# Performance work log

Measured on AMD Instinct MI355X. Metric: run time of the kernel, lower is better.

Reference implementation:

```python
import jax, jax.numpy as jnp
import numpy as np

MODEL_DIM = 1024
NUM_HEADS = 16
K_DIM = MODEL_DIM // NUM_HEADS


def setup_inputs() -> dict:
    key = jax.random.key(0)
    kx, kw1, kw2 = jax.random.split(key, 3)
    B, L, D = 4, 2048, MODEL_DIM
    x = jax.random.normal(kx, (B, L, D), dtype=jnp.float32)
    # nn.Linear(D, 3D, bias=False): y = x @ W^T; store transposed form [D, 3D]
    scale1 = 1.0 / np.sqrt(D)
    Wqkv = jax.random.uniform(kw1, (D, 3 * D), dtype=jnp.float32, minval=-scale1, maxval=scale1)
    Wout = jax.random.uniform(kw2, (D, D), dtype=jnp.float32, minval=-scale1, maxval=scale1)
    return {"x": x, "Wqkv": Wqkv, "Wout": Wout}


def reference(x, Wqkv, Wout):
    B, L, D = x.shape
    H, Kd = NUM_HEADS, K_DIM
    qkv = x @ Wqkv  # [B, L, 3D]
    q, k, v = jnp.split(qkv, 3, axis=-1)

    def heads(t):  # [B, L, D] -> [B, H, L, Kd]
        return t.reshape(B, L, H, Kd).transpose(0, 2, 1, 3)

    qh, kh, vh = heads(q), heads(k), heads(v)
    scores = jnp.einsum('bhqd,bhkd->bhqk', qh, kh) / jnp.sqrt(jnp.float32(Kd))
    causal = jnp.triu(jnp.ones((L, L), dtype=bool), k=1)  # True above diagonal
    scores = jnp.where(causal, -jnp.inf, scores)
    probs = jax.nn.softmax(scores, axis=-1)
    attended = jnp.einsum('bhqk,bhkd->bhqd', probs, vh)
    concatted = attended.transpose(0, 2, 1, 3).reshape(B, L, D)
    # dropout is identity in eval mode
    return concatted @ Wout
```

## Files before the change

kernel.cpp:

```cpp
#include <hip/hip_runtime.h>

typedef unsigned short u16;
typedef unsigned int   u32;
typedef __bf16   bf16x8 __attribute__((ext_vector_type(8)));
typedef float    f32x4  __attribute__((ext_vector_type(4)));
typedef u16      u16x4  __attribute__((ext_vector_type(4)));
typedef u16      u16x8  __attribute__((ext_vector_type(8)));
typedef u32      u32x2  __attribute__((ext_vector_type(2)));
typedef u32      u32x4  __attribute__((ext_vector_type(4)));

#if __has_builtin(__builtin_amdgcn_exp2f)
#define EXP2(x) __builtin_amdgcn_exp2f(x)
#else
#define EXP2(x) exp2f(x)
#endif

__device__ __forceinline__ u16 f2bf(float f) {
    unsigned u = __float_as_uint(f);
    u += 0x7FFFu + ((u >> 16) & 1u);
    return (u16)(u >> 16);
}

__device__ __forceinline__ u32 pack_bf16(float a, float b) {
#if __has_builtin(__builtin_amdgcn_cvt_pk_bf16_f32)
    typedef __bf16 bf16x2 __attribute__((ext_vector_type(2)));
    bf16x2 r = __builtin_amdgcn_cvt_pk_bf16_f32(a, b);
    return __builtin_bit_cast(u32, r);
#else
    return (u32)f2bf(a) | ((u32)f2bf(b) << 16);
#endif
}

__device__ __forceinline__ void async_copy16(const u16* g, u16* l) {
    __builtin_amdgcn_global_load_lds(
        (const __attribute__((address_space(1))) unsigned*)g,
        (__attribute__((address_space(3))) unsigned*)l, 16, 0, 0);
}

__device__ __forceinline__ bf16x8 lds_frag(const u16* p) {
    return *(const bf16x8*)p;
}

__device__ __forceinline__ void permlane32_swap(u32& a, u32& b) {
    asm("v_permlane32_swap_b32 %0, %1" : "+v"(a), "+v"(b));
}
__device__ __forceinline__ void permlane16_swap(u32& a, u32& b) {
    asm("v_permlane16_swap_b32 %0, %1" : "+v"(a), "+v"(b));
}

__global__ __launch_bounds__(256) void prep(const float* __restrict__ x,
                                            const float* __restrict__ Wqkv,
                                            const float* __restrict__ Wout,
                                            u16* __restrict__ xb,
                                            u16* __restrict__ wqkv_t,
                                            u16* __restrict__ wout_t) {
    __shared__ u16 t[64 * 72];
    const int bid = blockIdx.x;
    const int tid = threadIdx.x;

    if (bid >= 1024) {
        size_t i = ((size_t)(bid - 1024) * 256 + tid) * 8;
        float4 v0 = *(const float4*)(x + i);
        float4 v1 = *(const float4*)(x + i + 4);
        u16x8 o = { f2bf(v0.x), f2bf(v0.y), f2bf(v0.z), f2bf(v0.w),
                    f2bf(v1.x), f2bf(v1.y), f2bf(v1.z), f2bf(v1.w) };
        *(u16x8*)(xb + i) = o;
        return;
    }

    const float* W;  u16* Wt;  int Kd, Nd, n0, k0;
    if (bid < 768) { W = Wqkv; Wt = wqkv_t; Kd = 1024; Nd = 3072;
                     n0 = (bid % 48) * 64; k0 = (bid / 48) * 64; }
    else           { W = Wout; Wt = wout_t; Kd = 1024; Nd = 1024;
                     n0 = ((bid - 768) % 16) * 64; k0 = ((bid - 768) / 16) * 64; }
#pragma unroll
    for (int i = 0; i < 4; ++i) {
        int lin = i * 256 + tid;
        int kr = lin >> 4, nc = (lin & 15) << 2;
        float4 v = *(const float4*)(W + (size_t)(k0 + kr) * Nd + n0 + nc);
        u16x4 o = { f2bf(v.x), f2bf(v.y), f2bf(v.z), f2bf(v.w) };
        *(u16x4*)&t[kr * 72 + nc] = o;
    }
    __syncthreads();
#pragma unroll
    for (int i = 0; i < 2; ++i) {
        int lin = i * 256 + tid;
        int nr = lin >> 3, kc = (lin & 7) << 3;
        u16x8 o;
#pragma unroll
        for (int jj = 0; jj < 8; ++jj) o[jj] = t[(kc + jj) * 72 + nr];
        *(u16x8*)(Wt + (size_t)(n0 + nr) * Kd + k0 + kc) = o;
    }
}

__global__ __launch_bounds__(256) void gemm_qkv(const u16* __restrict__ A,
                                                const u16* __restrict__ Bt,
                                                u16* __restrict__ outb,
                                                int K, int N) {
    __shared__ u16 As[2][128 * 32];
    __shared__ u16 Bs[2][128 * 32];
    const int tid = threadIdx.x;
    const int lane = tid & 63;
    const int wv = tid >> 6;
    const int wr = (wv >> 1) * 64;
    const int wc = (wv & 1) * 64;
    const int qd = lane >> 4;
    const int c  = lane & 15;
    const int m0 = blockIdx.y * 128;
    const int n0 = blockIdx.x * 128;

    const int srow = tid >> 2;
    const int sg = ((tid & 3) ^ ((srow >> 1) & 3)) << 3;

    const u16* Ag0 = A  + (size_t)(m0 +      srow) * K + sg;
    const u16* Ag1 = A  + (size_t)(m0 + 64 + srow) * K + sg;
    const u16* Bg0 = Bt + (size_t)(n0 +      srow) * K + sg;
    const u16* Bg1 = Bt + (size_t)(n0 + 64 + srow) * K + sg;

    const u32 fsw = (qd ^ ((c >> 1) & 3)) << 3;
    const u32 a_off = (wr + c) * 32 + fsw;
    const u32 b_off = (wc + c) * 32 + fsw;

    f32x4 acc[4][4] = {};

    async_copy16(Ag0, &As[0][tid * 8]);
    async_copy16(Ag1, &As[0][2048 + tid * 8]);
    async_copy16(Bg0, &Bs[0][tid * 8]);
    async_copy16(Bg1, &Bs[0][2048 + tid * 8]);

    int p = 0;
    for (int k0 = 0; k0 < K; k0 += 32) {
        __syncthreads();
        if (k0 + 32 < K) {
            const int np = p ^ 1;
            async_copy16(Ag0 + k0 + 32, &As[np][tid * 8]);
            async_copy16(Ag1 + k0 + 32, &As[np][2048 + tid * 8]);
            async_copy16(Bg0 + k0 + 32, &Bs[np][tid * 8]);
            async_copy16(Bg1 + k0 + 32, &Bs[np][2048 + tid * 8]);
        }
        bf16x8 af[4], bfr[4];
#pragma unroll
        for (int i = 0; i < 4; ++i) af[i]  = lds_frag(&As[p][a_off + i * 512]);
#pragma unroll
        for (int j = 0; j < 4; ++j) bfr[j] = lds_frag(&Bs[p][b_off + j * 512]);
#pragma unroll
        for (int i = 0; i < 4; ++i)
#pragma unroll
            for (int j = 0; j < 4; ++j)
                acc[i][j] = __builtin_amdgcn_mfma_f32_16x16x32_bf16(af[i], bfr[j], acc[i][j], 0, 0, 0);
        p ^= 1;
    }

#pragma unroll
    for (int i = 0; i < 4; ++i)
#pragma unroll
        for (int j = 0; j < 4; ++j) {
            int n = n0 + wc + j * 16 + c;
            int which = n >> 10, h = (n >> 6) & 15, kd = n & 63;
            int m_base = m0 + wr + i * 16 + qd * 4;
            int b = m_base >> 11, l0 = m_base & 2047;
            int bh = b * 16 + h;
            if (which == 2) {
                u32x2 o2;
                o2[0] = pack_bf16(acc[i][j][0], acc[i][j][1]);
                o2[1] = pack_bf16(acc[i][j][2], acc[i][j][3]);
                *(u32x2*)(outb + (size_t)(128 + bh) * 131072 + (size_t)kd * 2048 + l0) = o2;
            } else if (which == 0) {
#pragma unroll
                for (int r = 0; r < 4; ++r)
                    outb[(size_t)bh * 131072 + (size_t)(l0 + r) * 64 + kd] =
                        f2bf(acc[i][j][r] * 0.1803368801f);
            } else {
#pragma unroll
                for (int r = 0; r < 4; ++r)
                    outb[(size_t)(64 + bh) * 131072 + (size_t)(l0 + r) * 64 + kd] =
                        f2bf(acc[i][j][r]);
            }
        }
}

__global__ __launch_bounds__(256) void gemm_out(const u16* __restrict__ A,
                                                const u16* __restrict__ Bt,
                                                float* __restrict__ outf,
                                                int K, int N) {
    __shared__ u16 As[2][64 * 32];
    __shared__ u16 Bs[2][128 * 32];
    const int tid = threadIdx.x;
    const int lane = tid & 63;
    const int wv = tid >> 6;
    const int wr = (wv >> 1) * 32;
    const int wc = (wv & 1) * 64;
    const int qd = lane >> 4;
    const int c  = lane & 15;
    const int m0 = blockIdx.y * 64;
    const int n0 = blockIdx.x * 128;

    const int srow = tid >> 2;
    const int sg = ((tid & 3) ^ ((srow >> 1) & 3)) << 3;

    const u16* Ag0 = A  + (size_t)(m0 +      srow) * K + sg;
    const u16* Bg0 = Bt + (size_t)(n0 +      srow) * K + sg;
    const u16* Bg1 = Bt + (size_t)(n0 + 64 + srow) * K + sg;

    const u32 fsw = (qd ^ ((c >> 1) & 3)) << 3;
    const u32 a_off = (wr + c) * 32 + fsw;
    const u32 b_off = (wc + c) * 32 + fsw;

    f32x4 acc[2][4] = {};

    async_copy16(Ag0, &As[0][tid * 8]);
    async_copy16(Bg0, &Bs[0][tid * 8]);
    async_copy16(Bg1, &Bs[0][2048 + tid * 8]);

    int p = 0;
    for (int k0 = 0; k0 < K; k0 += 32) {
        __syncthreads();
        if (k0 + 32 < K) {
            const int np = p ^ 1;
            async_copy16(Ag0 + k0 + 32, &As[np][tid * 8]);
            async_copy16(Bg0 + k0 + 32, &Bs[np][tid * 8]);
            async_copy16(Bg1 + k0 + 32, &Bs[np][2048 + tid * 8]);
        }
        bf16x8 af[2], bfr[4];
#pragma unroll
        for (int i = 0; i < 2; ++i) af[i]  = lds_frag(&As[p][a_off + i * 512]);
#pragma unroll
        for (int j = 0; j < 4; ++j) bfr[j] = lds_frag(&Bs[p][b_off + j * 512]);
#pragma unroll
        for (int i = 0; i < 2; ++i)
#pragma unroll
            for (int j = 0; j < 4; ++j)
                acc[i][j] = __builtin_amdgcn_mfma_f32_16x16x32_bf16(af[i], bfr[j], acc[i][j], 0, 0, 0);
        p ^= 1;
    }

#pragma unroll
    for (int i = 0; i < 2; ++i)
#pragma unroll
        for (int j = 0; j < 4; ++j)
#pragma unroll
            for (int r = 0; r < 4; ++r) {
                int m = m0 + wr + i * 16 + qd * 4 + r;
                int n = n0 + wc + j * 16 + c;
                outf[(size_t)m * N + n] = acc[i][j][r];
            }
}

#define ATTN_COMPUTE_S(KSB, QARR, S)                                          \
    do {                                                                      \
        _Pragma("unroll") for (int f = 0; f < 8; ++f)                         \
            S[f] = f32x4{-8.f, -8.f, -8.f, -8.f};                             \
        __builtin_amdgcn_s_setprio(1);                                        \
        _Pragma("unroll") for (int ks = 0; ks < 2; ++ks) {                    \
            const u16* kp = (KSB) + kf_off[ks];                               \
            _Pragma("unroll") for (int f = 0; f < 8; ++f) {                   \
                bf16x8 kf = lds_frag(kp + f * 1024);                          \
                S[f] = __builtin_amdgcn_mfma_f32_16x16x32_bf16(               \
                    kf, QARR[ks], S[f], 0, 0, 0);                             \
            }                                                                 \
        }                                                                     \
        __builtin_amdgcn_s_setprio(0);                                        \
    } while (0)

#define ATTN_FINISH(S, QROW, RV, ACC, VTB, KT)                                \
    do {                                                                      \
        if ((KT) == qt) {                                                     \
            _Pragma("unroll") for (int f = 0; f < 8; ++f)                     \
                _Pragma("unroll") for (int r = 0; r < 4; ++r) {               \
                    int key = (KT) * 128 + f * 16 + qd * 4 + r;               \
                    if (key > (QROW)) S[f][r] = -3e38f;                       \
                }                                                             \
        }                                                                     \
        _Pragma("unroll") for (int f = 0; f < 8; ++f) {                       \
            _Pragma("unroll") for (int r = 0; r < 4; ++r)                     \
                S[f][r] = EXP2(S[f][r]);                                      \
            RV += S[f];                                                       \
        }                                                                     \
        _Pragma("unroll") for (int kc = 0; kc < 4; ++kc) {                    \
            u32 a0 = pack_bf16(S[2 * kc][0], S[2 * kc][1]);                   \
            u32 a1 = pack_bf16(S[2 * kc + 1][0], S[2 * kc + 1][1]);           \
            u32 b0 = pack_bf16(S[2 * kc][2], S[2 * kc][3]);                   \
            u32 b1 = pack_bf16(S[2 * kc + 1][2], S[2 * kc + 1][3]);           \
            permlane32_swap(a0, a1); permlane16_swap(a0, a1);                 \
            permlane32_swap(b0, b1); permlane16_swap(b0, b1);                 \
            u32x4 wpk = {a0, b0, a1, b1};                                     \
            bf16x8 pfrag = __builtin_bit_cast(bf16x8, wpk);                   \
            const u16* vp = (VTB) + vf_off[kc];                               \
            __builtin_amdgcn_s_setprio(1);                                    \
            _Pragma("unroll") for (int jo = 0; jo < 4; ++jo) {                \
                bf16x8 vf = lds_frag(vp + jo * 2048);                         \
                ACC[jo] = __builtin_amdgcn_mfma_f32_16x16x32_bf16(            \
                    vf, pfrag, ACC[jo], 0, 0, 0);                             \
            }                                                                 \
            __builtin_amdgcn_s_setprio(0);                                    \
        }                                                                     \
    } while (0)

__global__ __launch_bounds__(256, 2) void attn_kernel(const u16* __restrict__ qkv,
                                                      u16* __restrict__ att) {
    __shared__ u16 Ks[2][128 * 64];
    __shared__ u16 Vt[3][64 * 128];

    const int tid = threadIdx.x;
    const int lane = tid & 63;
    const int w = tid >> 6;
    const int qd = lane >> 4;
    const int c = lane & 15;

    const int flat = blockIdx.x + 8 * blockIdx.y;
    const int bh = (flat & 7) + 8 * ((flat >> 3) & 7);
    const int bx = flat >> 6;
    const int b = bh >> 4, h = bh & 15;

    const u16* Qg = qkv + (size_t)bh * 131072;
    const u16* Kg = qkv + (size_t)(64 + bh) * 131072;
    const u16* Vg = qkv + (size_t)(128 + bh) * 131072;

    u32 kf_off[2];
#pragma unroll
    for (int ks = 0; ks < 2; ++ks)
        kf_off[ks] = c * 64 + (((ks * 4 + qd) ^ (c & 7)) << 3);
    u32 vf_off[4];
#pragma unroll
    for (int kc = 0; kc < 4; ++kc)
        vf_off[kc] = c * 128 + (((kc * 4 + qd) ^ c) << 3);

    auto issue_copy = [&](int t, u16* kd, u16* vd) {
#pragma unroll
        for (int it = 0; it < 4; ++it) {
            int lin = it * 256 + tid;
            int krw = lin >> 3, kch = lin & 7;
            int vrw = lin >> 4, vch = lin & 15;
            async_copy16(Kg + (size_t)t * 8192 + krw * 64 + ((kch ^ (krw & 7)) << 3),
                         kd + lin * 8);
            async_copy16(Vg + (size_t)t * 128 + (size_t)vrw * 2048 + ((vch ^ (vrw & 15)) << 3),
                         vd + lin * 8);
        }
    };

#pragma unroll 1
    for (int seg = 0; seg < 2; ++seg) {
        const int qt = seg ? (15 - bx) : bx;
        const int qa_row = qt * 128 + w * 32 + c;
        const int qb_row = qa_row + 16;

        bf16x8 qa[2], qb[2];
#pragma unroll
        for (int ks = 0; ks < 2; ++ks) {
            qa[ks] = *(const bf16x8*)(Qg + (size_t)qa_row * 64 + ks * 32 + qd * 8);
            qb[ks] = *(const bf16x8*)(Qg + (size_t)qb_row * 64 + ks * 32 + qd * 8);
        }

        f32x4 acca[4] = {}, accb[4] = {};
        f32x4 rva = {}, rvb = {};
        f32x4 sa[8], sb[8];

        const int nkt = qt + 1;

        __syncthreads();
        issue_copy(0, Ks[0], Vt[0]);
        __syncthreads();
        if (nkt > 1) issue_copy(1, Ks[1], Vt[1]);
        ATTN_COMPUTE_S(Ks[0], qa, sa);

        u16 *vPV = Vt[0], *vNx = Vt[1], *vFr = Vt[2];

#pragma unroll 1
        for (int kt = 0; kt < nkt; ++kt) {
            ATTN_COMPUTE_S(Ks[kt & 1], qb, sb);
            ATTN_FINISH(sa, qa_row, rva, acca, vPV, kt);
            if (kt + 1 < nkt) {
                __syncthreads();
                if (kt + 2 < nkt) issue_copy(kt + 2, Ks[kt & 1], vFr);
                ATTN_COMPUTE_S(Ks[(kt + 1) & 1], qa, sa);
            }
            ATTN_FINISH(sb, qb_row, rvb, accb, vPV, kt);
            u16* t0 = vPV; vPV = vNx; vNx = vFr; vFr = t0;
        }

        float ra = rva[0] + rva[1] + rva[2] + rva[3];
        float rb = rvb[0] + rvb[1] + rvb[2] + rvb[3];
        ra += __shfl_xor(ra, 16, 64);
        ra += __shfl_xor(ra, 32, 64);
        rb += __shfl_xor(rb, 16, 64);
        rb += __shfl_xor(rb, 32, 64);
        float ia = __builtin_amdgcn_rcpf(ra), ib = __builtin_amdgcn_rcpf(rb);
        u16* ar = att + ((size_t)b * 2048 + qa_row) * 1024 + h * 64;
        u16* br = att + ((size_t)b * 2048 + qb_row) * 1024 + h * 64;
#pragma unroll
        for (int jo = 0; jo < 4; ++jo) {
            u32x2 oa, ob;
            oa[0] = pack_bf16(acca[jo][0] * ia, acca[jo][1] * ia);
            oa[1] = pack_bf16(acca[jo][2] * ia, acca[jo][3] * ia);
            ob[0] = pack_bf16(accb[jo][0] * ib, accb[jo][1] * ib);
            ob[1] = pack_bf16(accb[jo][2] * ib, accb[jo][3] * ib);
            *(u32x2*)(ar + jo * 16 + qd * 4) = oa;
            *(u32x2*)(br + jo * 16 + qd * 4) = ob;
        }
    }
}

extern "C" void kernel_launch(void* const* d_in, const int* in_sizes, int n_in,
                              void* d_out, int out_size, void* d_ws, size_t ws_size,
                              hipStream_t stream) {
    const float* x    = (const float*)d_in[0];
    const float* Wqkv = (const float*)d_in[1];
    const float* Wout = (const float*)d_in[2];
    float* out = (float*)d_out;

    char* ws = (char*)d_ws;
    u16* x_bf   = (u16*)(ws);
    u16* wqkv_t = (u16*)(ws + 16777216);
    u16* wout_t = (u16*)(ws + 23068672);
    u16* qkv_h  = (u16*)(ws + 25165824);
    u16* att    = (u16*)(ws + 75497472);

    prep<<<dim3(5120), dim3(256), 0, stream>>>(x, Wqkv, Wout, x_bf, wqkv_t, wout_t);
    gemm_qkv<<<dim3(24, 64), dim3(256), 0, stream>>>(x_bf, wqkv_t, qkv_h, 1024, 3072);
    attn_kernel<<<dim3(8, 64), dim3(256), 0, stream>>>(qkv_h, att);
    gemm_out<<<dim3(8, 128), dim3(256), 0, stream>>>(att, wout_t, out, 1024, 1024);
}
```

Measured before the change: 250.3 us.

## Process both query tiles together per key tile and drop triple V buffer

Replaces the staggered software pipeline, where S for one query sub-tile was computed while the other's softmax/PV ran, with a single fused step that computes S for both query tiles off a shared K fragment load and then does exp/PV for both. Each K and V LDS fragment is now loaded once and used for two MFMAs. The V tile buffer drops from triple to double buffering, cutting LDS use. In exchange the MFMA/VALU interleaving from the staggered schedule is lost, and the single barrier per iteration now guards reuse of the same Ks/Vt buffer.

```diff
diff --git a/kernel.cpp b/kernel.cpp
--- a/kernel.cpp
+++ b/kernel.cpp
@@ -246,51 +246,69 @@
             }
 }
 
-#define ATTN_COMPUTE_S(KSB, QARR, S)                                          \
+#define ATTN_S_AB(KSB)                                                        \
     do {                                                                      \
-        _Pragma("unroll") for (int f = 0; f < 8; ++f)                         \
-            S[f] = f32x4{-8.f, -8.f, -8.f, -8.f};                             \
+        _Pragma("unroll") for (int f = 0; f < 8; ++f) {                       \
+            sa[f] = f32x4{-8.f, -8.f, -8.f, -8.f};                            \
+            sb[f] = f32x4{-8.f, -8.f, -8.f, -8.f};                            \
+        }                                                                     \
         __builtin_amdgcn_s_setprio(1);                                        \
         _Pragma("unroll") for (int ks = 0; ks < 2; ++ks) {                    \
             const u16* kp = (KSB) + kf_off[ks];                               \
             _Pragma("unroll") for (int f = 0; f < 8; ++f) {                   \
                 bf16x8 kf = lds_frag(kp + f * 1024);                          \
-                S[f] = __builtin_amdgcn_mfma_f32_16x16x32_bf16(               \
-                    kf, QARR[ks], S[f], 0, 0, 0);                             \
+                sa[f] = __builtin_amdgcn_mfma_f32_16x16x32_bf16(              \
+                    kf, qa[ks], sa[f], 0, 0, 0);                              \
+                sb[f] = __builtin_amdgcn_mfma_f32_16x16x32_bf16(              \
+                    kf, qb[ks], sb[f], 0, 0, 0);                              \
             }                                                                 \
         }                                                                     \
         __builtin_amdgcn_s_setprio(0);                                        \
     } while (0)
 
-#define ATTN_FINISH(S, QROW, RV, ACC, VTB, KT)                                \
+#define ATTN_FINISH_AB(VTB, KT)                                               \
     do {                                                                      \
         if ((KT) == qt) {                                                     \
             _Pragma("unroll") for (int f = 0; f < 8; ++f)                     \
                 _Pragma("unroll") for (int r = 0; r < 4; ++r) {               \
                     int key = (KT) * 128 + f * 16 + qd * 4 + r;               \
-                    if (key > (QROW)) S[f][r] = -3e38f;                       \
+                    if (key > qa_row) sa[f][r] = -3e38f;                      \
+                    if (key > qb_row) sb[f][r] = -3e38f;                      \
                 }                                                             \
         }                                                                     \
         _Pragma("unroll") for (int f = 0; f < 8; ++f) {                       \
-            _Pragma("unroll") for (int r = 0; r < 4; ++r)                     \
-                S[f][r] = EXP2(S[f][r]);                                      \
-            RV += S[f];                                                       \
+            _Pragma("unroll") for (int r = 0; r < 4; ++r) {                   \
+                sa[f][r] = EXP2(sa[f][r]);                                    \
+                sb[f][r] = EXP2(sb[f][r]);                                    \
+            }                                                                 \
+            rva += sa[f];                                                     \
+            rvb += sb[f];                                                     \
         }                                                                     \
         _Pragma("unroll") for (int kc = 0; kc < 4; ++kc) {                    \
-            u32 a0 = pack_bf16(S[2 * kc][0], S[2 * kc][1]);                   \
-            u32 a1 = pack_bf16(S[2 * kc + 1][0], S[2 * kc + 1][1]);           \
-            u32 b0 = pack_bf16(S[2 * kc][2], S[2 * kc][3]);                   \
-            u32 b1 = pack_bf16(S[2 * kc + 1][2], S[2 * kc + 1][3]);           \
+            u32 a0 = pack_bf16(sa[2 * kc][0], sa[2 * kc][1]);                 \
+            u32 a1 = pack_bf16(sa[2 * kc + 1][0], sa[2 * kc + 1][1]);         \
+            u32 b0 = pack_bf16(sa[2 * kc][2], sa[2 * kc][3]);                 \
+            u32 b1 = pack_bf16(sa[2 * kc + 1][2], sa[2 * kc + 1][3]);         \
             permlane32_swap(a0, a1); permlane16_swap(a0, a1);                 \
             permlane32_swap(b0, b1); permlane16_swap(b0, b1);                 \
-            u32x4 wpk = {a0, b0, a1, b1};                                     \
-            bf16x8 pfrag = __builtin_bit_cast(bf16x8, wpk);                   \
+            u32x4 wpa = {a0, b0, a1, b1};                                     \
+            bf16x8 pa = __builtin_bit_cast(bf16x8, wpa);                      \
+            u32 c0 = pack_bf16(sb[2 * kc][0], sb[2 * kc][1]);                 \
+            u32 c1 = pack_bf16(sb[2 * kc + 1][0], sb[2 * kc + 1][1]);         \
+            u32 d0 = pack_bf16(sb[2 * kc][2], sb[2 * kc][3]);                 \
+            u32 d1 = pack_bf16(sb[2 * kc + 1][2], sb[2 * kc + 1][3]);         \
+            permlane32_swap(c0, c1); permlane16_swap(c0, c1);                 \
+            permlane32_swap(d0, d1); permlane16_swap(d0, d1);                 \
+            u32x4 wpb = {c0, d0, c1, d1};                                     \
+            bf16x8 pb = __builtin_bit_cast(bf16x8, wpb);                      \
             const u16* vp = (VTB) + vf_off[kc];                               \
             __builtin_amdgcn_s_setprio(1);                                    \
             _Pragma("unroll") for (int jo = 0; jo < 4; ++jo) {                \
                 bf16x8 vf = lds_frag(vp + jo * 2048);                         \
-                ACC[jo] = __builtin_amdgcn_mfma_f32_16x16x32_bf16(            \
-                    vf, pfrag, ACC[jo], 0, 0, 0);                             \
+                acca[jo] = __builtin_amdgcn_mfma_f32_16x16x32_bf16(           \
+                    vf, pa, acca[jo], 0, 0, 0);                               \
+                accb[jo] = __builtin_amdgcn_mfma_f32_16x16x32_bf16(           \
+                    vf, pb, accb[jo], 0, 0, 0);                               \
             }                                                                 \
             __builtin_amdgcn_s_setprio(0);                                    \
         }                                                                     \
@@ -299,7 +317,7 @@
 __global__ __launch_bounds__(256, 2) void attn_kernel(const u16* __restrict__ qkv,
                                                       u16* __restrict__ att) {
     __shared__ u16 Ks[2][128 * 64];
-    __shared__ u16 Vt[3][64 * 128];
+    __shared__ u16 Vt[2][64 * 128];
 
     const int tid = threadIdx.x;
     const int lane = tid & 63;
@@ -361,21 +379,16 @@
         issue_copy(0, Ks[0], Vt[0]);
         __syncthreads();
         if (nkt > 1) issue_copy(1, Ks[1], Vt[1]);
-        ATTN_COMPUTE_S(Ks[0], qa, sa);
-
-        u16 *vPV = Vt[0], *vNx = Vt[1], *vFr = Vt[2];
 
 #pragma unroll 1
         for (int kt = 0; kt < nkt; ++kt) {
-            ATTN_COMPUTE_S(Ks[kt & 1], qb, sb);
-            ATTN_FINISH(sa, qa_row, rva, acca, vPV, kt);
+            const int p = kt & 1;
+            ATTN_S_AB(Ks[p]);
+            ATTN_FINISH_AB(Vt[p], kt);
             if (kt + 1 < nkt) {
                 __syncthreads();
-                if (kt + 2 < nkt) issue_copy(kt + 2, Ks[kt & 1], vFr);
-                ATTN_COMPUTE_S(Ks[(kt + 1) & 1], qa, sa);
+                if (kt + 2 < nkt) issue_copy(kt + 2, Ks[p], Vt[p]);
             }
-            ATTN_FINISH(sb, qb_row, rvb, accb, vPV, kt);
-            u16* t0 = vPV; vPV = vNx; vNx = vFr; vFr = t0;
         }
 
         float ra = rva[0] + rva[1] + rva[2] + rva[3];
```

Result: no change. 246.2 us (-1.7%).
